# Kernel optimization log

Measured on AMD Instinct MI355X. Metric: run time of the kernel, lower is better.

Reference implementation:

```python
import jax, jax.numpy as jnp
import numpy as np

DILATED = (1, 2, 3)
NUM_PROTOS = 100
PROTO_SIZE = 4
ENC_SIZE = 1600
NUM_CLASSES = 2
B, L = 64, 256

# num_filters split exactly as in torch: floor(P/len) each, first gets remainder
_nf = [NUM_PROTOS // len(DILATED)] * len(DILATED)
_nf[0] += NUM_PROTOS % len(DILATED)
NUM_FILTERS = tuple(_nf)  # (34, 33, 33)


def setup_inputs() -> dict:
    key = jax.random.key(0)
    k1, k2, k3 = jax.random.split(key, 3)
    embedding = jax.random.normal(k1, (B, L, ENC_SIZE), dtype=jnp.float32)
    # nn.init.uniform_ default is U[0,1)
    protolayer = jax.random.uniform(k2, (NUM_PROTOS, ENC_SIZE, PROTO_SIZE), dtype=jnp.float32)
    fc_w = jax.random.normal(k3, (NUM_CLASSES, NUM_PROTOS), dtype=jnp.float32) * 0.1
    return {"embedding": embedding, "protolayer": protolayer, "fc_w": fc_w}


def _l2_convolution(x_bel, protolayer):
    # x_bel: [B, L, E] -> [B, E, L] for NCH conv layout
    x = jnp.transpose(x_bel, (0, 2, 1))
    # sliding-window sum of x^2 computed ONCE per dilation (shared across protos,
    # mathematically identical to conv1d with all-ones weight)
    s = jnp.sum(x * x, axis=1)  # [B, L]
    p2_sum = jnp.sum(protolayer * protolayer, axis=(1, 2))  # [P]
    distances = []
    j = 0
    Lx = x.shape[2]
    for d, n in zip(DILATED, NUM_FILTERS):
        L_out = Lx - (PROTO_SIZE - 1) * d
        # windowed sum over K=PROTO_SIZE taps with dilation d: [B, L_out]
        x2_patch = sum(s[:, k * d:k * d + L_out] for k in range(PROTO_SIZE))
        # dilated cross-correlation x * p : [B, n, L_out]
        xp = jax.lax.conv_general_dilated(
            x, protolayer[j:j + n],
            window_strides=(1,), padding='VALID', rhs_dilation=(d,),
            dimension_numbers=('NCH', 'OIH', 'NCH'))
        dist = jnp.sqrt(jnp.abs(x2_patch[:, None, :] - 2.0 * xp
                                + p2_sum[j:j + n][None, :, None]))
        distances.append(dist)
        j += n
    return distances


def reference(embedding, protolayer, fc_w):
    distances = _l2_convolution(embedding, protolayer)
    prototype_distances = jnp.concatenate(
        [jnp.min(d, axis=2) for d in distances], axis=1)  # [B, P]
    class_out = prototype_distances @ fc_w.T  # [B, num_classes]
    return (prototype_distances, distances[0], distances[1], distances[2], class_out)
```

## Files before the change

kernel.cpp:

```cpp
#include <hip/hip_runtime.h>

#define B_   64
#define L_   256
#define E_   1600
#define P_   100
#define KP   4
#define N0 34
#define N1 33
#define N2 33
#define LOUT0 253
#define LOUT1 250
#define LOUT2 247
#define OFF_PD 0
#define OFF_D0 6400
#define OFF_D1 (OFF_D0 + B_*N0*LOUT0)
#define OFF_D2 (OFF_D1 + B_*N1*LOUT1)
#define OFF_CO (OFF_D2 + B_*N2*LOUT2)

#define WS_ABF  0ull
#define WS_BT   52428800ull
#define WS_S    (WS_BT + 1280000ull)
#define WS_P2   (WS_S + 65536ull)
#define WS_NEED (WS_P2 + 512ull)

#define TM   144
#define BKB  128
#define BOFF 18432

typedef float f32x4 __attribute__((ext_vector_type(4)));
typedef unsigned short ushort8v __attribute__((ext_vector_type(8)));
typedef __bf16 bf16x8 __attribute__((ext_vector_type(8)));
typedef _Float16 f16;

__device__ __forceinline__ unsigned short bf16rne(float f) {
    unsigned u = __float_as_uint(f);
    u += 0x7FFFu + ((u >> 16) & 1u);
    return (unsigned short)(u >> 16);
}

typedef __attribute__((address_space(3))) void lds_void_t;
typedef __attribute__((address_space(1))) void glb_void_t;

__device__ __forceinline__ void gload16(const void* g, void* l) {
    __builtin_amdgcn_global_load_lds((const glb_void_t*)g, (lds_void_t*)l, 16, 0, 0);
}


__global__ __launch_bounds__(256) void proto_prep_fast(
        const float* __restrict__ emb, const float* __restrict__ proto,
        char* __restrict__ ws, float* __restrict__ out) {
    int q = blockIdx.x;
    int wave = threadIdx.x >> 6, lane = threadIdx.x & 63;
    if (q < 4096) {
        int row = q * 4 + wave;
        const float4* r = (const float4*)(emb + (size_t)row * E_);
        unsigned short* dst = (unsigned short*)(ws + WS_ABF + (size_t)row * (E_*2));
        float acc = 0.f;
        #pragma unroll
        for (int it = 0; it < 6; ++it) {
            int e4 = it * 64 + lane;
            float4 v = r[e4];
            acc += v.x*v.x + v.y*v.y + v.z*v.z + v.w*v.w;
            ushort4 bv = make_ushort4(bf16rne(v.x), bf16rne(v.y),
                                      bf16rne(v.z), bf16rne(v.w));
            *(ushort4*)(dst + e4 * 4) = bv;
        }
        if (lane < 16) {
            int e4 = 384 + lane;
            float4 v = r[e4];
            acc += v.x*v.x + v.y*v.y + v.z*v.z + v.w*v.w;
            ushort4 bv = make_ushort4(bf16rne(v.x), bf16rne(v.y),
                                      bf16rne(v.z), bf16rne(v.w));
            *(ushort4*)(dst + e4 * 4) = bv;
        }
        #pragma unroll
        for (int off = 32; off; off >>= 1) acc += __shfl_down(acc, off);
        if (lane == 0) ((float*)(ws + WS_S))[row] = acc;
    } else if (q < 4121) {
        int p = (q - 4096) * 4 + wave;
        if (p < P_) {
            const float4* r = (const float4*)(proto + (size_t)p * (E_ * KP));
            unsigned short* bt = (unsigned short*)(ws + WS_BT);
            float acc = 0.f;
            #pragma unroll
            for (int it = 0; it < 25; ++it) {
                int e = it * 64 + lane;
                float4 v = r[e];
                acc += v.x*v.x + v.y*v.y + v.z*v.z + v.w*v.w;
                bt[(size_t)(4*p + 0) * E_ + e] = bf16rne(v.x);
                bt[(size_t)(4*p + 1) * E_ + e] = bf16rne(v.y);
                bt[(size_t)(4*p + 2) * E_ + e] = bf16rne(v.z);
                bt[(size_t)(4*p + 3) * E_ + e] = bf16rne(v.w);
            }
            #pragma unroll
            for (int off = 32; off; off >>= 1) acc += __shfl_down(acc, off);
            if (lane == 0) ((float*)(ws + WS_P2))[p] = acc;
        }
    } else {
        for (int i = threadIdx.x; i < B_ * P_; i += 256)
            out[OFF_PD + i] = __uint_as_float(0x7F800000u);
    }
}

__global__ __launch_bounds__(192, 4) void proto_main_fast(
        const char* __restrict__ ws, float* __restrict__ out) {

    __shared__ __align__(16) char smem[28672];

    int bx0 = blockIdx.x;
    int lb  = (bx0 & 7) * 80 + (bx0 >> 3);
    int b     = lb / 10;
    int inner = lb % 10;
    int m     = inner / 5;
    int n_blk = inner % 5;
    int r0    = m ? 112 : 0;
    int pbase = n_blk * 20;

    const char* Ag = ws + WS_ABF + (size_t)(b * L_ + r0) * (E_ * 2);
    const char* Bg = ws + WS_BT  + (size_t)(pbase * 4) * (E_ * 2);

    int tid  = threadIdx.x;
    int lane = tid & 63;
    int wave = tid >> 6;
    int mrow = lane & 15;
    int jq   = lane >> 4;
    int lrow8 = lane >> 3;
    int jst   = lane & 7;

    f32x4 acc[3][5] = {};

    for (int c = 0; c < 25; ++c) {
        int eoff = c * BKB;
        for (int t = wave; t < 28; t += 3) {
            if (t < 18) {
                int rowl = t * 8 + lrow8;
                int j = jst ^ (rowl & 7);
                gload16(Ag + (size_t)rowl * (E_*2) + eoff + j * 16,
                        smem + t * 1024);
            } else {
                int rowl = (t - 18) * 8 + lrow8;
                int j = jst ^ (rowl & 7);
                gload16(Bg + (size_t)rowl * (E_*2) + eoff + j * 16,
                        smem + BOFF + (t - 18) * 1024);
            }
        }
        __syncthreads();

        #pragma unroll
        for (int ks = 0; ks < 2; ++ks) {
            ushort8v af[3], bfv[5];
            #pragma unroll
            for (int mi = 0; mi < 3; ++mi) {
                int rowl = wave * 48 + mi * 16 + mrow;
                af[mi] = *(const ushort8v*)(smem + rowl * 128
                            + (((ks << 2) + jq) ^ (rowl & 7)) * 16);
            }
            #pragma unroll
            for (int ni = 0; ni < 5; ++ni) {
                int rown = ni * 16 + mrow;
                bfv[ni] = *(const ushort8v*)(smem + BOFF + rown * 128
                            + (((ks << 2) + jq) ^ (rown & 7)) * 16);
            }
            #pragma unroll
            for (int mi = 0; mi < 3; ++mi)
                #pragma unroll
                for (int ni = 0; ni < 5; ++ni)
                    acc[mi][ni] = __builtin_amdgcn_mfma_f32_16x16x32_bf16(
                        __builtin_bit_cast(bf16x8, af[mi]),
                        __builtin_bit_cast(bf16x8, bfv[ni]),
                        acc[mi][ni], 0, 0, 0);
        }
        __syncthreads();
    }

    f16*      Yh     = (f16*)smem;
    float*    slds   = (float*)(smem + 23328);
    float*    p2lds  = slds + TM;
    unsigned* minlds = (unsigned*)(p2lds + 20);

    {
        int colq = lane & 15;
        int rowq = (lane >> 4) * 4;
        #pragma unroll
        for (int mi = 0; mi < 3; ++mi) {
            int row = wave * 48 + mi * 16 + rowq;
            #pragma unroll
            for (int ni = 0; ni < 5; ++ni) {
                int col = ni * 16 + colq;
                #pragma unroll
                for (int r = 0; r < 4; ++r)
                    Yh[(row + r) * 81 + col] = (f16)acc[mi][ni][r];
            }
        }
    }
    if (tid < TM) slds[tid] = ((const float*)(ws + WS_S))[b * L_ + r0 + tid];
    if (tid < 20) {
        p2lds[tid] = ((const float*)(ws + WS_P2))[pbase + tid];
        minlds[tid] = 0x7F800000u;
    }
    __syncthreads();

    int l_lo = m * 128;
    for (int idx = tid; idx < 20 * 128; idx += 192) {
        int pl  = idx >> 7;
        int lof = idx & 127;
        int p = pbase + pl;
        int d, Lout, nseg, pseg; size_t segbase;
        if (p < 34)      { d = 1; Lout = LOUT0; segbase = OFF_D0; pseg = p;      nseg = N0; }
        else if (p < 67) { d = 2; Lout = LOUT1; segbase = OFF_D1; pseg = p - 34; nseg = N1; }
        else             { d = 3; Lout = LOUT2; segbase = OFF_D2; pseg = p - 67; nseg = N2; }
        int l = l_lo + lof;
        if (l < Lout) {
            int rl = l - r0;
            int c0 = pl * 4;
            float xp = (float)Yh[rl * 81 + c0]
                     + (float)Yh[(rl + d) * 81 + c0 + 1]
                     + (float)Yh[(rl + 2*d) * 81 + c0 + 2]
                     + (float)Yh[(rl + 3*d) * 81 + c0 + 3];
            float x2 = slds[rl] + slds[rl + d] + slds[rl + 2*d] + slds[rl + 3*d];
            float dist = sqrtf(fabsf(x2 - 2.f * xp + p2lds[pl]));
            out[segbase + ((size_t)b * nseg + pseg) * Lout + l] = dist;
            atomicMin(&minlds[pl], __float_as_uint(dist));
        }
    }
    __syncthreads();
    if (tid < 20)
        atomicMin((unsigned*)out + OFF_PD + b * P_ + pbase + tid, minlds[tid]);
}

#define ASTR 40
#define YSTR 81

__global__ __launch_bounds__(256) void proto_prep_kernel(
        const float* __restrict__ emb, const float* __restrict__ proto,
        float* __restrict__ ws_s, float* __restrict__ ws_p2,
        float* __restrict__ out) {
    int q = blockIdx.x;
    int wave = threadIdx.x >> 6, lane = threadIdx.x & 63;
    if (q < 4096) {
        int row = q * 4 + wave;
        const float4* r = (const float4*)(emb + (size_t)row * E_);
        float acc = 0.f;
        #pragma unroll
        for (int it = 0; it < 7; ++it) {
            int e4 = it * 64 + lane;
            if (e4 < 400) {
                float4 v = r[e4];
                acc += v.x*v.x + v.y*v.y + v.z*v.z + v.w*v.w;
            }
        }
        #pragma unroll
        for (int off = 32; off; off >>= 1) acc += __shfl_down(acc, off);
        if (lane == 0) ws_s[row] = acc;
    } else if (q < 4121) {
        int p = (q - 4096) * 4 + wave;
        if (p < P_) {
            const float4* r = (const float4*)(proto + (size_t)p * (E_ * KP));
            float acc = 0.f;
            #pragma unroll
            for (int it = 0; it < 25; ++it) {
                float4 v = r[it * 64 + lane];
                acc += v.x*v.x + v.y*v.y + v.z*v.z + v.w*v.w;
            }
            #pragma unroll
            for (int off = 32; off; off >>= 1) acc += __shfl_down(acc, off);
            if (lane == 0) ws_p2[p] = acc;
        }
    } else {
        for (int i = threadIdx.x; i < B_ * P_; i += 256)
            out[OFF_PD + i] = __uint_as_float(0x7F800000u);
    }
}

__global__ __launch_bounds__(192) void proto_main_kernel(
        const float* __restrict__ emb, const float* __restrict__ proto,
        const float* __restrict__ ws_s, const float* __restrict__ ws_p2,
        float* __restrict__ out) {

    __shared__ __align__(16) char smem[47392];
    unsigned short* Ald = (unsigned short*)smem;
    unsigned short* Bld = (unsigned short*)(smem + TM*ASTR*2);

    int bx = blockIdx.x;
    int n_blk = bx % 5;
    int m     = (bx / 5) & 1;
    int b     = bx / 10;
    int r0    = m ? 112 : 0;
    int pbase = n_blk * 20;

    const float* Abase = emb + ((size_t)(b * L_ + r0)) * E_;
    const float* Bbase = proto + (size_t)pbase * (E_ * KP);

    int tid  = threadIdx.x;
    int lane = tid & 63;
    int wave = tid >> 6;
    int mrow = lane & 15;
    int kq   = (lane >> 4) * 8;

    f32x4 acc[3][5] = {};

    for (int c = 0; c < E_ / 32; ++c) {
        int e0 = c * 32;
        #pragma unroll
        for (int i = 0; i < 6; ++i) {
            int idx = tid + i * 192;
            int row = idx >> 3;
            int e4  = idx & 7;
            float4 v = *(const float4*)(Abase + (size_t)row * E_ + e0 + e4 * 4);
            ushort4 bv = make_ushort4(bf16rne(v.x), bf16rne(v.y),
                                      bf16rne(v.z), bf16rne(v.w));
            *(ushort4*)&Ald[row * ASTR + e4 * 4] = bv;
        }
        for (int idx = tid; idx < 640; idx += 192) {
            int pl = idx >> 5;
            int el = idx & 31;
            float4 v = *(const float4*)(Bbase + (size_t)pl * (E_ * KP)
                                        + (size_t)(e0 + el) * KP);
            Bld[(4*pl + 0) * ASTR + el] = bf16rne(v.x);
            Bld[(4*pl + 1) * ASTR + el] = bf16rne(v.y);
            Bld[(4*pl + 2) * ASTR + el] = bf16rne(v.z);
            Bld[(4*pl + 3) * ASTR + el] = bf16rne(v.w);
        }
        __syncthreads();

        ushort8v af[3], bfr[5];
        #pragma unroll
        for (int mi = 0; mi < 3; ++mi)
            af[mi] = *(const ushort8v*)&Ald[(wave*48 + mi*16 + mrow) * ASTR + kq];
        #pragma unroll
        for (int ni = 0; ni < 5; ++ni)
            bfr[ni] = *(const ushort8v*)&Bld[(ni*16 + mrow) * ASTR + kq];
        #pragma unroll
        for (int mi = 0; mi < 3; ++mi)
            #pragma unroll
            for (int ni = 0; ni < 5; ++ni)
                acc[mi][ni] = __builtin_amdgcn_mfma_f32_16x16x32_bf16(
                    __builtin_bit_cast(bf16x8, af[mi]),
                    __builtin_bit_cast(bf16x8, bfr[ni]),
                    acc[mi][ni], 0, 0, 0);
        __syncthreads();
    }

    float*    Ylds   = (float*)smem;
    float*    slds   = (float*)(smem + TM * YSTR * 4);
    float*    p2lds  = slds + TM;
    unsigned* minlds = (unsigned*)(p2lds + 20);

    {
        int colq = lane & 15;
        int rowq = (lane >> 4) * 4;
        #pragma unroll
        for (int mi = 0; mi < 3; ++mi) {
            int row = wave * 48 + mi * 16 + rowq;
            #pragma unroll
            for (int ni = 0; ni < 5; ++ni) {
                int col = ni * 16 + colq;
                #pragma unroll
                for (int r = 0; r < 4; ++r)
                    Ylds[(row + r) * YSTR + col] = acc[mi][ni][r];
            }
        }
    }
    if (tid < TM) slds[tid] = ws_s[b * L_ + r0 + tid];
    if (tid < 20) { p2lds[tid] = ws_p2[pbase + tid]; minlds[tid] = 0x7F800000u; }
    __syncthreads();

    int l_lo = m * 128;
    for (int idx = tid; idx < 20 * 128; idx += 192) {
        int pl  = idx >> 7;
        int lof = idx & 127;
        int p = pbase + pl;
        int d, Lout, nseg, pseg; size_t segbase;
        if (p < 34)      { d = 1; Lout = LOUT0; segbase = OFF_D0; pseg = p;      nseg = N0; }
        else if (p < 67) { d = 2; Lout = LOUT1; segbase = OFF_D1; pseg = p - 34; nseg = N1; }
        else             { d = 3; Lout = LOUT2; segbase = OFF_D2; pseg = p - 67; nseg = N2; }
        int l = l_lo + lof;
        if (l < Lout) {
            int rl = l - r0;
            int c0 = pl * 4;
            float xp = Ylds[rl * YSTR + c0]
                     + Ylds[(rl + d) * YSTR + c0 + 1]
                     + Ylds[(rl + 2*d) * YSTR + c0 + 2]
                     + Ylds[(rl + 3*d) * YSTR + c0 + 3];
            float x2 = slds[rl] + slds[rl + d] + slds[rl + 2*d] + slds[rl + 3*d];
            float dist = sqrtf(fabsf(x2 - 2.f * xp + p2lds[pl]));
            out[segbase + ((size_t)b * nseg + pseg) * Lout + l] = dist;
            atomicMin(&minlds[pl], __float_as_uint(dist));
        }
    }
    __syncthreads();
    if (tid < 20)
        atomicMin((unsigned*)out + OFF_PD + b * P_ + pbase + tid, minlds[tid]);
}

__global__ __launch_bounds__(128) void proto_fc_kernel(
        const float* __restrict__ fc_w, float* __restrict__ out) {
    int t = threadIdx.x;
    int b = t >> 1, c = t & 1;
    const float* pd = out + OFF_PD + b * P_;
    const float* w  = fc_w + c * P_;
    float s = 0.f;
    #pragma unroll 4
    for (int p = 0; p < P_; ++p) s += pd[p] * w[p];
    out[OFF_CO + b * 2 + c] = s;
}

extern "C" void kernel_launch(void* const* d_in, const int* in_sizes, int n_in,
                              void* d_out, int out_size, void* d_ws, size_t ws_size,
                              hipStream_t stream) {
    const float* emb   = (const float*)d_in[0];
    const float* proto = (const float*)d_in[1];
    const float* fc_w  = (const float*)d_in[2];
    float* out  = (float*)d_out;

    if (ws_size >= WS_NEED) {
        char* ws = (char*)d_ws;
        proto_prep_fast<<<4122, 256, 0, stream>>>(emb, proto, ws, out);
        proto_main_fast<<<640, 192, 0, stream>>>(ws, out);
    } else {
        float* ws_s  = (float*)d_ws;
        float* ws_p2 = ws_s + B_ * L_;
        proto_prep_kernel<<<4122, 256, 0, stream>>>(emb, proto, ws_s, ws_p2, out);
        proto_main_kernel<<<640, 192, 0, stream>>>(emb, proto, ws_s, ws_p2, out);
    }
    proto_fc_kernel<<<1, 128, 0, stream>>>(fc_w, out);
}
```

Before: 218.8 us.

## Split main GEMM into three row tiles with six waves each

```diff
diff --git a/kernel.cpp b/kernel.cpp
--- a/kernel.cpp
+++ b/kernel.cpp
@@ -23,9 +23,9 @@
 #define WS_P2   (WS_S + 65536ull)
 #define WS_NEED (WS_P2 + 512ull)
 
-#define TM   144
+#define TMF  96
 #define BKB  128
-#define BOFF 18432
+#define BOFF2 12288
 
 typedef float f32x4 __attribute__((ext_vector_type(4)));
 typedef unsigned short ushort8v __attribute__((ext_vector_type(8)));
@@ -102,108 +102,100 @@
     }
 }
 
-__global__ __launch_bounds__(192, 4) void proto_main_fast(
+__global__ __launch_bounds__(384, 6) void proto_main_fast(
         const char* __restrict__ ws, float* __restrict__ out) {
 
-    __shared__ __align__(16) char smem[28672];
-
-    int bx0 = blockIdx.x;
-    int lb  = (bx0 & 7) * 80 + (bx0 >> 3);
-    int b     = lb / 10;
-    int inner = lb % 10;
+    __shared__ __align__(16) char smem[22528];
+
+    int bx   = blockIdx.x;
+    int lb   = (bx & 7) * 120 + (bx >> 3);
+    int b     = lb / 15;
+    int inner = lb % 15;
     int m     = inner / 5;
     int n_blk = inner % 5;
-    int r0    = m ? 112 : 0;
+    int r0    = (m == 0) ? 0 : (m == 1 ? 87 : 160);
+    int l_lo  = m * 87;
     int pbase = n_blk * 20;
 
     const char* Ag = ws + WS_ABF + (size_t)(b * L_ + r0) * (E_ * 2);
     const char* Bg = ws + WS_BT  + (size_t)(pbase * 4) * (E_ * 2);
 
-    int tid  = threadIdx.x;
-    int lane = tid & 63;
-    int wave = tid >> 6;
-    int mrow = lane & 15;
-    int jq   = lane >> 4;
+    int tid   = threadIdx.x;
+    int lane  = tid & 63;
+    int wave  = tid >> 6;
+    int mrow  = lane & 15;
+    int jq    = lane >> 4;
     int lrow8 = lane >> 3;
     int jst   = lane & 7;
 
-    f32x4 acc[3][5] = {};
+    f32x4 acc[5] = {};
 
     for (int c = 0; c < 25; ++c) {
         int eoff = c * BKB;
-        for (int t = wave; t < 28; t += 3) {
-            if (t < 18) {
+        for (int t = wave; t < 22; t += 6) {
+            if (t < 12) {
                 int rowl = t * 8 + lrow8;
                 int j = jst ^ (rowl & 7);
                 gload16(Ag + (size_t)rowl * (E_*2) + eoff + j * 16,
                         smem + t * 1024);
             } else {
-                int rowl = (t - 18) * 8 + lrow8;
+                int rowl = (t - 12) * 8 + lrow8;
                 int j = jst ^ (rowl & 7);
                 gload16(Bg + (size_t)rowl * (E_*2) + eoff + j * 16,
-                        smem + BOFF + (t - 18) * 1024);
+                        smem + BOFF2 + (t - 12) * 1024);
             }
         }
         __syncthreads();
 
         #pragma unroll
         for (int ks = 0; ks < 2; ++ks) {
-            ushort8v af[3], bfv[5];
-            #pragma unroll
-            for (int mi = 0; mi < 3; ++mi) {
-                int rowl = wave * 48 + mi * 16 + mrow;
-                af[mi] = *(const ushort8v*)(smem + rowl * 128
-                            + (((ks << 2) + jq) ^ (rowl & 7)) * 16);
-            }
+            int rowA = wave * 16 + mrow;
+            ushort8v af = *(const ushort8v*)(smem + rowA * 128
+                            + (((ks << 2) + jq) ^ (rowA & 7)) * 16);
+            ushort8v bfv[5];
             #pragma unroll
             for (int ni = 0; ni < 5; ++ni) {
-                int rown = ni * 16 + mrow;
-                bfv[ni] = *(const ushort8v*)(smem + BOFF + rown * 128
-                            + (((ks << 2) + jq) ^ (rown & 7)) * 16);
-            }
-            #pragma unroll
-            for (int mi = 0; mi < 3; ++mi)
-                #pragma unroll
-                for (int ni = 0; ni < 5; ++ni)
-                    acc[mi][ni] = __builtin_amdgcn_mfma_f32_16x16x32_bf16(
-                        __builtin_bit_cast(bf16x8, af[mi]),
-                        __builtin_bit_cast(bf16x8, bfv[ni]),
-                        acc[mi][ni], 0, 0, 0);
+                int rowB = ni * 16 + mrow;
+                bfv[ni] = *(const ushort8v*)(smem + BOFF2 + rowB * 128
+                            + (((ks << 2) + jq) ^ (rowB & 7)) * 16);
+            }
+            #pragma unroll
+            for (int ni = 0; ni < 5; ++ni)
+                acc[ni] = __builtin_amdgcn_mfma_f32_16x16x32_bf16(
+                    __builtin_bit_cast(bf16x8, af),
+                    __builtin_bit_cast(bf16x8, bfv[ni]),
+                    acc[ni], 0, 0, 0);
         }
         __syncthreads();
     }
 
     f16*      Yh     = (f16*)smem;
-    float*    slds   = (float*)(smem + 23328);
-    float*    p2lds  = slds + TM;
+    float*    slds   = (float*)(smem + 15552);
+    float*    p2lds  = slds + TMF;
     unsigned* minlds = (unsigned*)(p2lds + 20);
 
     {
         int colq = lane & 15;
         int rowq = (lane >> 4) * 4;
-        #pragma unroll
-        for (int mi = 0; mi < 3; ++mi) {
-            int row = wave * 48 + mi * 16 + rowq;
-            #pragma unroll
-            for (int ni = 0; ni < 5; ++ni) {
-                int col = ni * 16 + colq;
-                #pragma unroll
-                for (int r = 0; r < 4; ++r)
-                    Yh[(row + r) * 81 + col] = (f16)acc[mi][ni][r];
-            }
-        }
-    }
-    if (tid < TM) slds[tid] = ((const float*)(ws + WS_S))[b * L_ + r0 + tid];
+        int row = wave * 16 + rowq;
+        #pragma unroll
+        for (int ni = 0; ni < 5; ++ni) {
+            int col = ni * 16 + colq;
+            #pragma unroll
+            for (int r = 0; r < 4; ++r)
+                Yh[(row + r) * 81 + col] = (f16)acc[ni][r];
+        }
+    }
+    if (tid < TMF) slds[tid] = ((const float*)(ws + WS_S))[b * L_ + r0 + tid];
     if (tid < 20) {
         p2lds[tid] = ((const float*)(ws + WS_P2))[pbase + tid];
         minlds[tid] = 0x7F800000u;
     }
     __syncthreads();
 
-    int l_lo = m * 128;
-    for (int idx = tid; idx < 20 * 128; idx += 192) {
-        int pl  = idx >> 7;
-        int lof = idx & 127;
+    for (int idx = tid; idx < 20 * 87; idx += 384) {
+        int pl  = idx / 87;
+        int lof = idx % 87;
         int p = pbase + pl;
         int d, Lout, nseg, pseg; size_t segbase;
         if (p < 34)      { d = 1; Lout = LOUT0; segbase = OFF_D0; pseg = p;      nseg = N0; }
@@ -228,6 +220,7 @@
         atomicMin((unsigned*)out + OFF_PD + b * P_ + pbase + tid, minlds[tid]);
 }
 
+#define TM   144
 #define ASTR 40
 #define YSTR 81
 
@@ -416,7 +409,7 @@
     if (ws_size >= WS_NEED) {
         char* ws = (char*)d_ws;
         proto_prep_fast<<<4122, 256, 0, stream>>>(emb, proto, ws, out);
-        proto_main_fast<<<640, 192, 0, stream>>>(ws, out);
+        proto_main_fast<<<960, 384, 0, stream>>>(ws, out);
     } else {
         float* ws_s  = (float*)d_ws;
         float* ws_p2 = ws_s + B_ * L_;
```

Measured after the change: 212.3 us. 2.9% less time.

## Prefetch next K-chunk into registers instead of direct global-to-LDS loads

Applied to the files above, without the earlier changes.

```diff
diff --git a/kernel.cpp b/kernel.cpp
--- a/kernel.cpp
+++ b/kernel.cpp
@@ -23,12 +23,12 @@
 #define WS_P2   (WS_S + 65536ull)
 #define WS_NEED (WS_P2 + 512ull)
 
-#define TM   144
-#define BKB  128
-#define BOFF 18432
+#define TM2   144
+#define BOFF3 18432
 
 typedef float f32x4 __attribute__((ext_vector_type(4)));
 typedef unsigned short ushort8v __attribute__((ext_vector_type(8)));
+typedef unsigned int uint4v __attribute__((ext_vector_type(4)));
 typedef __bf16 bf16x8 __attribute__((ext_vector_type(8)));
 typedef _Float16 f16;
 
@@ -36,13 +36,6 @@
     unsigned u = __float_as_uint(f);
     u += 0x7FFFu + ((u >> 16) & 1u);
     return (unsigned short)(u >> 16);
-}
-
-typedef __attribute__((address_space(3))) void lds_void_t;
-typedef __attribute__((address_space(1))) void glb_void_t;
-
-__device__ __forceinline__ void gload16(const void* g, void* l) {
-    __builtin_amdgcn_global_load_lds((const glb_void_t*)g, (lds_void_t*)l, 16, 0, 0);
 }
 
 
@@ -102,13 +95,13 @@
     }
 }
 
-__global__ __launch_bounds__(192, 4) void proto_main_fast(
+__global__ __launch_bounds__(192, 3) void proto_main_dbuf(
         const char* __restrict__ ws, float* __restrict__ out) {
 
     __shared__ __align__(16) char smem[28672];
 
-    int bx0 = blockIdx.x;
-    int lb  = (bx0 & 7) * 80 + (bx0 >> 3);
+    int bx    = blockIdx.x;
+    int lb    = (bx & 7) * 80 + (bx >> 3);
     int b     = lb / 10;
     int inner = lb % 10;
     int m     = inner / 5;
@@ -124,42 +117,63 @@
     int wave = tid >> 6;
     int mrow = lane & 15;
     int jq   = lane >> 4;
-    int lrow8 = lane >> 3;
-    int jst   = lane & 7;
+
+    int ag_off[6], al_off[6];
+    #pragma unroll
+    for (int i = 0; i < 6; ++i) {
+        int f = i * 192 + tid;
+        int row = f >> 3, slot = f & 7;
+        ag_off[i] = row * 3200 + slot * 16;
+        al_off[i] = row * 128 + ((slot ^ (row & 7)) * 16);
+    }
+    int bg_off[4], bl_off[4];
+    bool bok[4];
+    #pragma unroll
+    for (int j = 0; j < 4; ++j) {
+        int f = j * 192 + tid;
+        bok[j] = (f < 640);
+        int row = f >> 3, slot = f & 7;
+        bg_off[j] = row * 3200 + slot * 16;
+        bl_off[j] = row * 128 + ((slot ^ (row & 7)) * 16);
+    }
+
+    uint4v pa[6], pb[4];
+    #pragma unroll
+    for (int i = 0; i < 6; ++i) pa[i] = *(const uint4v*)(Ag + ag_off[i]);
+    #pragma unroll
+    for (int j = 0; j < 4; ++j) if (bok[j]) pb[j] = *(const uint4v*)(Bg + bg_off[j]);
 
     f32x4 acc[3][5] = {};
 
     for (int c = 0; c < 25; ++c) {
-        int eoff = c * BKB;
-        for (int t = wave; t < 28; t += 3) {
-            if (t < 18) {
-                int rowl = t * 8 + lrow8;
-                int j = jst ^ (rowl & 7);
-                gload16(Ag + (size_t)rowl * (E_*2) + eoff + j * 16,
-                        smem + t * 1024);
-            } else {
-                int rowl = (t - 18) * 8 + lrow8;
-                int j = jst ^ (rowl & 7);
-                gload16(Bg + (size_t)rowl * (E_*2) + eoff + j * 16,
-                        smem + BOFF + (t - 18) * 1024);
-            }
+        #pragma unroll
+        for (int i = 0; i < 6; ++i) *(uint4v*)(smem + al_off[i]) = pa[i];
+        #pragma unroll
+        for (int j = 0; j < 4; ++j) if (bok[j]) *(uint4v*)(smem + BOFF3 + bl_off[j]) = pb[j];
+        if (c < 24) {
+            int e = (c + 1) * 128;
+            #pragma unroll
+            for (int i = 0; i < 6; ++i) pa[i] = *(const uint4v*)(Ag + ag_off[i] + e);
+            #pragma unroll
+            for (int j = 0; j < 4; ++j) if (bok[j]) pb[j] = *(const uint4v*)(Bg + bg_off[j] + e);
         }
         __syncthreads();
 
         #pragma unroll
         for (int ks = 0; ks < 2; ++ks) {
-            ushort8v af[3], bfv[5];
+            ushort8v af[3];
             #pragma unroll
             for (int mi = 0; mi < 3; ++mi) {
-                int rowl = wave * 48 + mi * 16 + mrow;
-                af[mi] = *(const ushort8v*)(smem + rowl * 128
-                            + (((ks << 2) + jq) ^ (rowl & 7)) * 16);
-            }
+                int rowA = wave * 48 + mi * 16 + mrow;
+                af[mi] = *(const ushort8v*)(smem + rowA * 128
+                            + (((ks << 2) + jq) ^ (rowA & 7)) * 16);
+            }
+            ushort8v bfv[5];
             #pragma unroll
             for (int ni = 0; ni < 5; ++ni) {
-                int rown = ni * 16 + mrow;
-                bfv[ni] = *(const ushort8v*)(smem + BOFF + rown * 128
-                            + (((ks << 2) + jq) ^ (rown & 7)) * 16);
+                int rowB = ni * 16 + mrow;
+                bfv[ni] = *(const ushort8v*)(smem + BOFF3 + rowB * 128
+                            + (((ks << 2) + jq) ^ (rowB & 7)) * 16);
             }
             #pragma unroll
             for (int mi = 0; mi < 3; ++mi)
@@ -175,8 +189,8 @@
 
     f16*      Yh     = (f16*)smem;
     float*    slds   = (float*)(smem + 23328);
-    float*    p2lds  = slds + TM;
-    unsigned* minlds = (unsigned*)(p2lds + 20);
+    float*    p2lds  = (float*)(smem + 23328 + 144*4);
+    unsigned* minlds = (unsigned*)(smem + 23328 + 144*4 + 80);
 
     {
         int colq = lane & 15;
@@ -193,7 +207,7 @@
             }
         }
     }
-    if (tid < TM) slds[tid] = ((const float*)(ws + WS_S))[b * L_ + r0 + tid];
+    if (tid < TM2) slds[tid] = ((const float*)(ws + WS_S))[b * L_ + r0 + tid];
     if (tid < 20) {
         p2lds[tid] = ((const float*)(ws + WS_P2))[pbase + tid];
         minlds[tid] = 0x7F800000u;
@@ -228,6 +242,7 @@
         atomicMin((unsigned*)out + OFF_PD + b * P_ + pbase + tid, minlds[tid]);
 }
 
+#define TM   144
 #define ASTR 40
 #define YSTR 81
 
@@ -416,7 +431,7 @@
     if (ws_size >= WS_NEED) {
         char* ws = (char*)d_ws;
         proto_prep_fast<<<4122, 256, 0, stream>>>(emb, proto, ws, out);
-        proto_main_fast<<<640, 192, 0, stream>>>(ws, out);
+        proto_main_dbuf<<<640, 192, 0, stream>>>(ws, out);
     } else {
         float* ws_s  = (float*)d_ws;
         float* ws_p2 = ws_s + B_ * L_;
```

Result: no change. 219.8 us (+0.5%).

## Fuse embedding bf16 conversion and squared-norm into main GEMM kernel

Applied to the files above, without the earlier changes.

```diff
diff --git a/kernel.cpp b/kernel.cpp
--- a/kernel.cpp
+++ b/kernel.cpp
@@ -17,17 +17,15 @@
 #define OFF_D2 (OFF_D1 + B_*N1*LOUT1)
 #define OFF_CO (OFF_D2 + B_*N2*LOUT2)
 
-#define WS_ABF  0ull
-#define WS_BT   52428800ull
-#define WS_S    (WS_BT + 1280000ull)
-#define WS_P2   (WS_S + 65536ull)
+#define WS_BT   0ull
+#define WS_P2   1280000ull
 #define WS_NEED (WS_P2 + 512ull)
 
-#define TM   144
-#define BKB  128
-#define BOFF 18432
+#define TM2   144
+#define BOFF4 36864
 
 typedef float f32x4 __attribute__((ext_vector_type(4)));
+typedef float f32x8 __attribute__((ext_vector_type(8)));
 typedef unsigned short ushort8v __attribute__((ext_vector_type(8)));
 typedef __bf16 bf16x8 __attribute__((ext_vector_type(8)));
 typedef _Float16 f16;
@@ -46,69 +44,43 @@
 }
 
 
-__global__ __launch_bounds__(256) void proto_prep_fast(
-        const float* __restrict__ emb, const float* __restrict__ proto,
-        char* __restrict__ ws, float* __restrict__ out) {
+__global__ __launch_bounds__(256) void proto_prepB_fast(
+        const float* __restrict__ proto, char* __restrict__ ws,
+        float* __restrict__ out) {
     int q = blockIdx.x;
     int wave = threadIdx.x >> 6, lane = threadIdx.x & 63;
-    if (q < 4096) {
-        int row = q * 4 + wave;
-        const float4* r = (const float4*)(emb + (size_t)row * E_);
-        unsigned short* dst = (unsigned short*)(ws + WS_ABF + (size_t)row * (E_*2));
+    if (q < 25) {
+        int p = q * 4 + wave;
+        const float4* r = (const float4*)(proto + (size_t)p * (E_ * KP));
+        unsigned short* bt = (unsigned short*)(ws + WS_BT);
         float acc = 0.f;
         #pragma unroll
-        for (int it = 0; it < 6; ++it) {
-            int e4 = it * 64 + lane;
-            float4 v = r[e4];
+        for (int it = 0; it < 25; ++it) {
+            int e = it * 64 + lane;
+            float4 v = r[e];
             acc += v.x*v.x + v.y*v.y + v.z*v.z + v.w*v.w;
-            ushort4 bv = make_ushort4(bf16rne(v.x), bf16rne(v.y),
-                                      bf16rne(v.z), bf16rne(v.w));
-            *(ushort4*)(dst + e4 * 4) = bv;
-        }
-        if (lane < 16) {
-            int e4 = 384 + lane;
-            float4 v = r[e4];
-            acc += v.x*v.x + v.y*v.y + v.z*v.z + v.w*v.w;
-            ushort4 bv = make_ushort4(bf16rne(v.x), bf16rne(v.y),
-                                      bf16rne(v.z), bf16rne(v.w));
-            *(ushort4*)(dst + e4 * 4) = bv;
+            bt[(size_t)(4*p + 0) * E_ + e] = bf16rne(v.x);
+            bt[(size_t)(4*p + 1) * E_ + e] = bf16rne(v.y);
+            bt[(size_t)(4*p + 2) * E_ + e] = bf16rne(v.z);
+            bt[(size_t)(4*p + 3) * E_ + e] = bf16rne(v.w);
         }
         #pragma unroll
         for (int off = 32; off; off >>= 1) acc += __shfl_down(acc, off);
-        if (lane == 0) ((float*)(ws + WS_S))[row] = acc;
-    } else if (q < 4121) {
-        int p = (q - 4096) * 4 + wave;
-        if (p < P_) {
-            const float4* r = (const float4*)(proto + (size_t)p * (E_ * KP));
-            unsigned short* bt = (unsigned short*)(ws + WS_BT);
-            float acc = 0.f;
-            #pragma unroll
-            for (int it = 0; it < 25; ++it) {
-                int e = it * 64 + lane;
-                float4 v = r[e];
-                acc += v.x*v.x + v.y*v.y + v.z*v.z + v.w*v.w;
-                bt[(size_t)(4*p + 0) * E_ + e] = bf16rne(v.x);
-                bt[(size_t)(4*p + 1) * E_ + e] = bf16rne(v.y);
-                bt[(size_t)(4*p + 2) * E_ + e] = bf16rne(v.z);
-                bt[(size_t)(4*p + 3) * E_ + e] = bf16rne(v.w);
-            }
-            #pragma unroll
-            for (int off = 32; off; off >>= 1) acc += __shfl_down(acc, off);
-            if (lane == 0) ((float*)(ws + WS_P2))[p] = acc;
-        }
+        if (lane == 0) ((float*)(ws + WS_P2))[p] = acc;
     } else {
         for (int i = threadIdx.x; i < B_ * P_; i += 256)
             out[OFF_PD + i] = __uint_as_float(0x7F800000u);
     }
 }
 
-__global__ __launch_bounds__(192, 4) void proto_main_fast(
-        const char* __restrict__ ws, float* __restrict__ out) {
-
-    __shared__ __align__(16) char smem[28672];
-
-    int bx0 = blockIdx.x;
-    int lb  = (bx0 & 7) * 80 + (bx0 >> 3);
+__global__ __launch_bounds__(192, 4) void proto_main_f32(
+        const float* __restrict__ emb, const char* __restrict__ ws,
+        float* __restrict__ out) {
+
+    __shared__ __align__(16) char smem[47104];
+
+    int bx    = blockIdx.x;
+    int lb    = (bx & 7) * 80 + (bx >> 3);
     int b     = lb / 10;
     int inner = lb % 10;
     int m     = inner / 5;
@@ -116,50 +88,61 @@
     int r0    = m ? 112 : 0;
     int pbase = n_blk * 20;
 
-    const char* Ag = ws + WS_ABF + (size_t)(b * L_ + r0) * (E_ * 2);
-    const char* Bg = ws + WS_BT  + (size_t)(pbase * 4) * (E_ * 2);
+    const char* Ag = (const char*)(emb + (size_t)(b * L_ + r0) * E_);
+    const char* Bg = ws + WS_BT + (size_t)(pbase * 4) * 3200;
 
     int tid  = threadIdx.x;
     int lane = tid & 63;
     int wave = tid >> 6;
     int mrow = lane & 15;
     int jq   = lane >> 4;
-    int lrow8 = lane >> 3;
-    int jst   = lane & 7;
+    int a_lr = lane >> 4;
+    int a_sl = lane & 15;
+    int b_lr = lane >> 3;
+    int b_sl = lane & 7;
 
     f32x4 acc[3][5] = {};
+    float sacc[3] = {0.f, 0.f, 0.f};
 
     for (int c = 0; c < 25; ++c) {
-        int eoff = c * BKB;
-        for (int t = wave; t < 28; t += 3) {
-            if (t < 18) {
-                int rowl = t * 8 + lrow8;
-                int j = jst ^ (rowl & 7);
-                gload16(Ag + (size_t)rowl * (E_*2) + eoff + j * 16,
-                        smem + t * 1024);
-            } else {
-                int rowl = (t - 18) * 8 + lrow8;
-                int j = jst ^ (rowl & 7);
-                gload16(Bg + (size_t)rowl * (E_*2) + eoff + j * 16,
-                        smem + BOFF + (t - 18) * 1024);
-            }
+        const char* Ac = Ag + c * 256;
+        const char* Bc = Bg + c * 128;
+
+        for (int t = wave; t < 10; t += 3) {
+            int row = t * 8 + b_lr;
+            gload16(Bc + (size_t)row * 3200 + ((b_sl ^ (row & 7)) * 16),
+                    smem + BOFF4 + t * 1024);
+        }
+        for (int t = wave; t < 36; t += 3) {
+            int row = t * 4 + a_lr;
+            gload16(Ac + (size_t)row * 6400 + ((a_sl ^ (row & 15)) * 16),
+                    smem + t * 1024);
         }
         __syncthreads();
 
         #pragma unroll
         for (int ks = 0; ks < 2; ++ks) {
-            ushort8v af[3], bfv[5];
+            ushort8v af[3];
             #pragma unroll
             for (int mi = 0; mi < 3; ++mi) {
-                int rowl = wave * 48 + mi * 16 + mrow;
-                af[mi] = *(const ushort8v*)(smem + rowl * 128
-                            + (((ks << 2) + jq) ^ (rowl & 7)) * 16);
-            }
+                int r  = wave * 48 + mi * 16 + mrow;
+                int s0 = ks * 8 + jq * 2;
+                f32x4 f0 = *(const f32x4*)(smem + r * 256 + ((s0 ^ (r & 15)) * 16));
+                f32x4 f1 = *(const f32x4*)(smem + r * 256 + (((s0 + 1) ^ (r & 15)) * 16));
+                sacc[mi] += f0[0]*f0[0] + f0[1]*f0[1] + f0[2]*f0[2] + f0[3]*f0[3]
+                          + f1[0]*f1[0] + f1[1]*f1[1] + f1[2]*f1[2] + f1[3]*f1[3];
+                f32x8 fv;
+                fv[0]=f0[0]; fv[1]=f0[1]; fv[2]=f0[2]; fv[3]=f0[3];
+                fv[4]=f1[0]; fv[5]=f1[1]; fv[6]=f1[2]; fv[7]=f1[3];
+                af[mi] = __builtin_bit_cast(ushort8v,
+                            __builtin_convertvector(fv, bf16x8));
+            }
+            ushort8v bfv[5];
             #pragma unroll
             for (int ni = 0; ni < 5; ++ni) {
-                int rown = ni * 16 + mrow;
-                bfv[ni] = *(const ushort8v*)(smem + BOFF + rown * 128
-                            + (((ks << 2) + jq) ^ (rown & 7)) * 16);
+                int rowB = ni * 16 + mrow;
+                bfv[ni] = *(const ushort8v*)(smem + BOFF4 + rowB * 128
+                            + (((ks << 2) + jq) ^ (rowB & 7)) * 16);
             }
             #pragma unroll
             for (int mi = 0; mi < 3; ++mi)
@@ -175,8 +158,8 @@
 
     f16*      Yh     = (f16*)smem;
     float*    slds   = (float*)(smem + 23328);
-    float*    p2lds  = slds + TM;
-    unsigned* minlds = (unsigned*)(p2lds + 20);
+    float*    p2lds  = (float*)(smem + 23328 + 576);
+    unsigned* minlds = (unsigned*)(smem + 23328 + 656);
 
     {
         int colq = lane & 15;
@@ -193,7 +176,18 @@
             }
         }
     }
-    if (tid < TM) slds[tid] = ((const float*)(ws + WS_S))[b * L_ + r0 + tid];
+    #pragma unroll
+    for (int mi = 0; mi < 3; ++mi) {
+        float v = sacc[mi];
+        v += __shfl_xor(v, 16);
+        v += __shfl_xor(v, 32);
+        sacc[mi] = v;
+    }
+    if (jq == 0) {
+        #pragma unroll
+        for (int mi = 0; mi < 3; ++mi)
+            slds[wave * 48 + mi * 16 + mrow] = sacc[mi];
+    }
     if (tid < 20) {
         p2lds[tid] = ((const float*)(ws + WS_P2))[pbase + tid];
         minlds[tid] = 0x7F800000u;
@@ -228,6 +222,7 @@
         atomicMin((unsigned*)out + OFF_PD + b * P_ + pbase + tid, minlds[tid]);
 }
 
+#define TM   144
 #define ASTR 40
 #define YSTR 81
 
@@ -415,8 +410,8 @@
 
     if (ws_size >= WS_NEED) {
         char* ws = (char*)d_ws;
-        proto_prep_fast<<<4122, 256, 0, stream>>>(emb, proto, ws, out);
-        proto_main_fast<<<640, 192, 0, stream>>>(ws, out);
+        proto_prepB_fast<<<26, 256, 0, stream>>>(proto, ws, out);
+        proto_main_f32<<<640, 192, 0, stream>>>(emb, ws, out);
     } else {
         float* ws_s  = (float*)d_ws;
         float* ws_p2 = ws_s + B_ * L_;
```

Measured after the change: 215.8 us. Within noise of the previous version (-1.3%).
